# Performance work log

Measured on AMD Instinct MI355X. Metric: run time of the kernel, lower is better.

The kernel has to match this reference:

```python
import jax, jax.numpy as jnp
import numpy as np

T, B, IN, H = 1024, 128, 256, 512


def setup_inputs() -> dict:
    key = jax.random.key(0)
    k1, k2, k3, k4, k5 = jax.random.split(key, 5)
    s = 1.0 / np.sqrt(H)  # PyTorch LSTM init scale
    return {
        "x": jax.random.normal(k1, (T, B, IN), dtype=jnp.float32),
        "W_ih": jax.random.normal(k2, (4 * H, IN), dtype=jnp.float32) * s,
        "W_hh": jax.random.normal(k3, (4 * H, H), dtype=jnp.float32) * s,
        "b_ih": jax.random.normal(k4, (4 * H,), dtype=jnp.float32) * s,
        "b_hh": jax.random.normal(k5, (4 * H,), dtype=jnp.float32) * s,
    }


def reference(x, W_ih, W_hh, b_ih, b_hh):
    # Single-layer unidirectional LSTM scanned over the full sequence.
    # PyTorch gate order within the 4H dim: i, f, g, o.
    b = b_ih + b_hh
    Wx = jnp.einsum('tbi,gi->tbg', x, W_ih) + b  # precompute input projection [T,B,4H]

    def step(carry, zx):
        h, c = carry
        z = zx + h @ W_hh.T  # [B, 4H]
        i, f, g, o = jnp.split(z, 4, axis=-1)
        i = jax.nn.sigmoid(i)
        f = jax.nn.sigmoid(f)
        g = jnp.tanh(g)
        o = jax.nn.sigmoid(o)
        c = f * c + i * g
        h = o * jnp.tanh(c)
        return (h, c), None

    h0 = jnp.zeros((B, H), dtype=x.dtype)
    c0 = jnp.zeros((B, H), dtype=x.dtype)
    (h, c), _ = jax.lax.scan(step, (h0, c0), Wx)
    # Original returns the LAST step's output plus (h_n, c_n); with 1 layer output == h_n.
    output = h[None]          # [1, B, H]
    h_n = h[None]             # [num_layers=1, B, H]
    c_n = c[None]
    return (output, h_n, c_n)
```

## Files before the change

kernel.cpp:

```cpp
#include <hip/hip_runtime.h>
#include <hip/hip_bf16.h>

typedef __attribute__((ext_vector_type(8)))  short short8;
typedef __attribute__((ext_vector_type(16))) float f32x16;
typedef __attribute__((ext_vector_type(4)))  unsigned int uint4v;

#define TSTEPS 1024
#define BATCH  128
#define NIN    256
#define NHID   512
#define GM     4
#define GHB    16
#define MBLK   32
#define NHB    32
#define XSTR   264
#define HSTR   520

__device__ __forceinline__ unsigned short f2bf(float f) {
  unsigned int u = __builtin_bit_cast(unsigned int, f);
  u += 0x7fffu + ((u >> 16) & 1u);
  return (unsigned short)(u >> 16);
}

__device__ __forceinline__ unsigned long long pack4(float a, float b, float c, float d) {
  return (unsigned long long)f2bf(a)
       | ((unsigned long long)f2bf(b) << 16)
       | ((unsigned long long)f2bf(c) << 32)
       | ((unsigned long long)f2bf(d) << 48);
}

__device__ __forceinline__ float sigf(float x) {
  return 1.0f / (1.0f + __expf(-x));
}
__device__ __forceinline__ float tanh_fast(float x) {
  x = fminf(fmaxf(x, -15.0f), 15.0f);
  float e = __expf(2.0f * x);
  return (e - 1.0f) / (e + 1.0f);
}

__global__ void init_ws_kernel(unsigned long long* hbuf, unsigned int* flags) {
  int idx = blockIdx.x * blockDim.x + threadIdx.x;
  if (idx < 16384) hbuf[idx] = 0ull;
  if (idx < 8192) flags[idx] = 0u;
}

#define MFMA(va, fb, acc) \
  acc = __builtin_amdgcn_mfma_f32_32x32x16_bf16(va, fb, acc, 0, 0, 0)
#define AFRAG(base, kb) (*(const short8*)((base) + ((((kb) ^ x2) << 4) + (h5 << 3))))

__global__ __launch_bounds__(256, 1) void lstm_persistent(
    const float* __restrict__ x,
    const float* __restrict__ Wih,
    const float* __restrict__ Whh,
    const float* __restrict__ bih,
    const float* __restrict__ bhh,
    float* __restrict__ out,
    unsigned long long* __restrict__ hbuf,
    unsigned int* __restrict__ flags)
{
  const int tid  = threadIdx.x;
  const int lane = tid & 63;
  const int wv   = tid >> 6;
  const int gm   = blockIdx.x & (GM - 1);
  const int gh   = blockIdx.x >> 2;
  const int m0   = gm * MBLK;
  const int hc0  = gh * NHB;

  __shared__ short x_lds[2][MBLK][XSTR];
  __shared__ short h_lds[2][MBLK][HSTR];
  __shared__ float z_lds[4][MBLK][36];

  const int ncol = lane & 31;
  const int kg   = (lane >> 5) * 8;
  const int gate = ncol >> 3;
  const int wrow = gate * NHID + hc0 + wv * 8 + (ncol & 7);

  short8 bfrag[48];
#pragma unroll
  for (int kb = 0; kb < 48; ++kb) {
    const float* src = (kb < 16)
        ? (Wih + (size_t)wrow * NIN  + (kb * 16 + kg))
        : (Whh + (size_t)wrow * NHID + (kb * 16 + kg - NIN));
    float4 f0 = *(const float4*)src;
    float4 f1 = *(const float4*)(src + 4);
    short8 b;
    b[0] = (short)f2bf(f0.x); b[1] = (short)f2bf(f0.y);
    b[2] = (short)f2bf(f0.z); b[3] = (short)f2bf(f0.w);
    b[4] = (short)f2bf(f1.x); b[5] = (short)f2bf(f1.y);
    b[6] = (short)f2bf(f1.z); b[7] = (short)f2bf(f1.w);
    bfrag[kb] = b;
  }
  const float bias_c = bih[wrow] + bhh[wrow];

  const int h5   = lane >> 5;
  const int x2   = (lane >> 3) & 3;
  const int arow = lane & 31;
  const int grow = lane >> 1;
  const int gcol = (lane & 1) * 4;
  float creg[4] = {0.0f, 0.0f, 0.0f, 0.0f};

  unsigned int* fgrp   = flags + gm * (64 * 32);
  unsigned int* myflag = fgrp + (gh * 4 + wv) * 32;

#define XLOAD(i, v) { int u = tid + 256 * (i); \
    v = *(const float4*)(xt + (size_t)(u >> 6) * NIN + (u & 63) * 4); }
#define XPACK(s, i, v) { int u = tid + 256 * (i); int r = u >> 6; int hc = u & 63; \
    int off = ((((hc >> 1) ^ (((r >> 3) & 3) << 1))) << 3) + ((hc & 1) << 2); \
    *(unsigned long long*)&x_lds[s][r][off] = pack4(v.x, v.y, v.z, v.w); }

  f32x16 a0, a1, a2, a3;
  float4 xv0, xv1, xv2, xv3, xv4, xv5, xv6, xv7;

  {
    const float* xt = x + (size_t)m0 * NIN;
    XLOAD(0, xv0) XLOAD(1, xv1) XLOAD(2, xv2) XLOAD(3, xv3)
    XLOAD(4, xv4) XLOAD(5, xv5) XLOAD(6, xv6) XLOAD(7, xv7)
    XPACK(0, 0, xv0) XPACK(0, 1, xv1) XPACK(0, 2, xv2) XPACK(0, 3, xv3)
    XPACK(0, 4, xv4) XPACK(0, 5, xv5) XPACK(0, 6, xv6) XPACK(0, 7, xv7)
  }
  __syncthreads();
  {
    const float* xt = x + ((size_t)BATCH + m0) * NIN;
    XLOAD(0, xv0) XLOAD(1, xv1) XLOAD(2, xv2) XLOAD(3, xv3)
    XLOAD(4, xv4) XLOAD(5, xv5) XLOAD(6, xv6) XLOAD(7, xv7)
  }
  a0 = (f32x16)bias_c;
  a1 = (f32x16)0.0f; a2 = (f32x16)0.0f; a3 = (f32x16)0.0f;
  {
    const short* xrow = &x_lds[0][arow][0];
#pragma unroll
    for (int kb = 0; kb < 16; kb += 4) {
      MFMA(AFRAG(xrow, kb + 0), bfrag[kb + 0], a0);
      MFMA(AFRAG(xrow, kb + 1), bfrag[kb + 1], a1);
      MFMA(AFRAG(xrow, kb + 2), bfrag[kb + 2], a2);
      MFMA(AFRAG(xrow, kb + 3), bfrag[kb + 3], a3);
    }
  }
  XPACK(1, 0, xv0) XPACK(1, 1, xv1) XPACK(1, 2, xv2) XPACK(1, 3, xv3)
  XPACK(1, 4, xv4) XPACK(1, 5, xv5) XPACK(1, 6, xv6) XPACK(1, 7, xv7)

  for (int t = 0; t < TSTEPS; ++t) {
    if (t > 0) {
      const unsigned int* fp = fgrp + lane * 32;
      unsigned int v = __hip_atomic_load(fp, __ATOMIC_RELAXED, __HIP_MEMORY_SCOPE_AGENT);
      while (!__all((int)(v >= (unsigned int)t))) {
        v = __hip_atomic_load(fp, __ATOMIC_RELAXED, __HIP_MEMORY_SCOPE_AGENT);
      }
    }

    {
      const char* p =
          (const char*)(hbuf + (size_t)(t & 1) * 16384 + (size_t)m0 * 128) + tid * 16;
      uint4v hv0, hv1, hv2, hv3, hv4, hv5, hv6, hv7;
      asm volatile("global_load_dwordx4 %0, %1, off sc0 sc1" : "=v"(hv0) : "v"(p + 0 * 4096));
      asm volatile("global_load_dwordx4 %0, %1, off sc0 sc1" : "=v"(hv1) : "v"(p + 1 * 4096));
      asm volatile("global_load_dwordx4 %0, %1, off sc0 sc1" : "=v"(hv2) : "v"(p + 2 * 4096));
      asm volatile("global_load_dwordx4 %0, %1, off sc0 sc1" : "=v"(hv3) : "v"(p + 3 * 4096));
      asm volatile("global_load_dwordx4 %0, %1, off sc0 sc1" : "=v"(hv4) : "v"(p + 4 * 4096));
      asm volatile("global_load_dwordx4 %0, %1, off sc0 sc1" : "=v"(hv5) : "v"(p + 5 * 4096));
      asm volatile("global_load_dwordx4 %0, %1, off sc0 sc1" : "=v"(hv6) : "v"(p + 6 * 4096));
      asm volatile("global_load_dwordx4 %0, %1, off sc0 sc1" : "=v"(hv7) : "v"(p + 7 * 4096));
      asm volatile("s_waitcnt vmcnt(0)" ::: "memory");
      __builtin_amdgcn_sched_barrier(0);
#pragma unroll
      for (int i = 0; i < 8; ++i) {
        int r   = wv + 4 * i;
        int c16 = lane ^ (((r >> 3) & 3) << 1);
        uint4v v = (i == 0) ? hv0 : (i == 1) ? hv1 : (i == 2) ? hv2 : (i == 3) ? hv3
                 : (i == 4) ? hv4 : (i == 5) ? hv5 : (i == 6) ? hv6 : hv7;
        *(uint4v*)&h_lds[t & 1][r][c16 << 3] = v;
      }
    }
    __syncthreads();

    if (t + 2 < TSTEPS) {
      const float* xt = x + ((size_t)(t + 2) * BATCH + m0) * NIN;
      XLOAD(0, xv0) XLOAD(1, xv1) XLOAD(2, xv2) XLOAD(3, xv3)
      XLOAD(4, xv4) XLOAD(5, xv5) XLOAD(6, xv6) XLOAD(7, xv7)
    }

    {
      const short* hrow = &h_lds[t & 1][arow][0];
#pragma unroll
      for (int kb = 0; kb < 32; kb += 4) {
        MFMA(AFRAG(hrow, kb + 0), bfrag[16 + kb + 0], a0);
        MFMA(AFRAG(hrow, kb + 1), bfrag[16 + kb + 1], a1);
        MFMA(AFRAG(hrow, kb + 2), bfrag[16 + kb + 2], a2);
        MFMA(AFRAG(hrow, kb + 3), bfrag[16 + kb + 3], a3);
      }
    }

    {
      f32x16 acc = (a0 + a1) + (a2 + a3);
#pragma unroll
      for (int r = 0; r < 16; ++r) {
        int zr = (r & 3) + 8 * (r >> 2) + 4 * h5;
        z_lds[wv][zr][ncol] = acc[r];
      }
      asm volatile("s_waitcnt lgkmcnt(0)" ::: "memory");
      const float* zrow = &z_lds[wv][grow][0];
      float4 vi = *(const float4*)&zrow[ 0 + gcol];
      float4 vf = *(const float4*)&zrow[ 8 + gcol];
      float4 vg = *(const float4*)&zrow[16 + gcol];
      float4 vo = *(const float4*)&zrow[24 + gcol];
      float zi[4] = {vi.x, vi.y, vi.z, vi.w};
      float zf[4] = {vf.x, vf.y, vf.z, vf.w};
      float zg[4] = {vg.x, vg.y, vg.z, vg.w};
      float zo[4] = {vo.x, vo.y, vo.z, vo.w};
      float hnv[4];
#pragma unroll
      for (int u = 0; u < 4; ++u) {
        float iv = sigf(zi[u]);
        float fv = sigf(zf[u]);
        float gv = tanh_fast(zg[u]);
        float ov = sigf(zo[u]);
        float cn = fv * creg[u] + iv * gv;
        creg[u] = cn;
        hnv[u] = ov * tanh_fast(cn);
      }
      if (t == TSTEPS - 1) {
        size_t o = (size_t)(m0 + grow) * NHID + hc0 + wv * 8 + gcol;
        float4 hq; hq.x = hnv[0]; hq.y = hnv[1]; hq.z = hnv[2]; hq.w = hnv[3];
        float4 cq; cq.x = creg[0]; cq.y = creg[1]; cq.z = creg[2]; cq.w = creg[3];
        *(float4*)&out[o]          = hq;
        *(float4*)&out[65536 + o]  = hq;
        *(float4*)&out[131072 + o] = cq;
      } else {
        unsigned long long hp = pack4(hnv[0], hnv[1], hnv[2], hnv[3]);
        size_t hoff = (size_t)((t + 1) & 1) * 16384
                    + (size_t)(m0 + grow) * 128 + (hc0 + wv * 8 + gcol) / 4;
        __hip_atomic_store(hbuf + hoff, hp, __ATOMIC_RELAXED, __HIP_MEMORY_SCOPE_AGENT);
        asm volatile("s_waitcnt vmcnt(0)" ::: "memory");
        if (lane == 0) {
          __hip_atomic_store(myflag, (unsigned int)(t + 1),
                             __ATOMIC_RELAXED, __HIP_MEMORY_SCOPE_AGENT);
        }
      }
    }

    if (t + 2 < TSTEPS) {
      XPACK(t & 1, 0, xv0) XPACK(t & 1, 1, xv1) XPACK(t & 1, 2, xv2) XPACK(t & 1, 3, xv3)
      XPACK(t & 1, 4, xv4) XPACK(t & 1, 5, xv5) XPACK(t & 1, 6, xv6) XPACK(t & 1, 7, xv7)
    }

    if (t < TSTEPS - 1) {
      a0 = (f32x16)bias_c;
      a1 = (f32x16)0.0f; a2 = (f32x16)0.0f; a3 = (f32x16)0.0f;
      const short* xrow = &x_lds[(t + 1) & 1][arow][0];
#pragma unroll
      for (int kb = 0; kb < 16; kb += 4) {
        MFMA(AFRAG(xrow, kb + 0), bfrag[kb + 0], a0);
        MFMA(AFRAG(xrow, kb + 1), bfrag[kb + 1], a1);
        MFMA(AFRAG(xrow, kb + 2), bfrag[kb + 2], a2);
        MFMA(AFRAG(xrow, kb + 3), bfrag[kb + 3], a3);
      }
    }
  }
#undef XLOAD
#undef XPACK
}

extern "C" void kernel_launch(void* const* d_in, const int* in_sizes, int n_in,
                              void* d_out, int out_size, void* d_ws, size_t ws_size,
                              hipStream_t stream) {
  const float* x   = (const float*)d_in[0];
  const float* Wih = (const float*)d_in[1];
  const float* Whh = (const float*)d_in[2];
  const float* bih = (const float*)d_in[3];
  const float* bhh = (const float*)d_in[4];
  float* out = (float*)d_out;

  unsigned long long* hbuf = (unsigned long long*)d_ws;
  unsigned int* flags = (unsigned int*)((char*)d_ws + 262144);

  hipLaunchKernelGGL(init_ws_kernel, dim3(64), dim3(256), 0, stream, hbuf, flags);
  hipLaunchKernelGGL(lstm_persistent, dim3(64), dim3(256), 0, stream,
                     x, Wih, Whh, bih, bhh, out, hbuf, flags);
}
```

Baseline: 4.105 ms.

## Pre-convert x to bf16 and stream it into LDS with async DMA

Adds a pre-pass that converts x to bf16 in workspace, then loads each timestep's x tile straight into LDS with global_load_lds, using a triple buffer and a prefetch distance of three steps. This removes the per-step fp32 loads, register staging and bf16 packing from the recurrent loop. The gate nonlinearity is also remapped across all 256 threads, with a block barrier after the z write, and the LDS swizzles are dropped for plain strided layouts. Costs: an extra full pass over x, a new __syncthreads per step, and possible LDS bank conflicts from removing the swizzle.

```diff
diff --git a/kernel.cpp b/kernel.cpp
--- a/kernel.cpp
+++ b/kernel.cpp
@@ -10,11 +10,11 @@
 #define NIN    256
 #define NHID   512
 #define GM     4
-#define GHB    16
 #define MBLK   32
-#define NHB    32
-#define XSTR   264
+#define XPSTR  528
+#define XBUF   8448
 #define HSTR   520
+#define HBUF   16640
 
 __device__ __forceinline__ unsigned short f2bf(float f) {
   unsigned int u = __builtin_bit_cast(unsigned int, f);
@@ -44,12 +44,21 @@
   if (idx < 8192) flags[idx] = 0u;
 }
 
+__global__ void convert_x_kernel(const float* __restrict__ x, unsigned short* __restrict__ xbf) {
+  const int N4 = TSTEPS * BATCH * NIN / 4;
+  for (int i = blockIdx.x * blockDim.x + threadIdx.x; i < N4; i += gridDim.x * blockDim.x) {
+    float4 f = *(const float4*)(x + (size_t)i * 4);
+    *(unsigned long long*)(xbf + (size_t)i * 4) = pack4(f.x, f.y, f.z, f.w);
+  }
+}
+
 #define MFMA(va, fb, acc) \
   acc = __builtin_amdgcn_mfma_f32_32x32x16_bf16(va, fb, acc, 0, 0, 0)
-#define AFRAG(base, kb) (*(const short8*)((base) + ((((kb) ^ x2) << 4) + (h5 << 3))))
-
+
+template <int USE_DMA>
 __global__ __launch_bounds__(256, 1) void lstm_persistent(
     const float* __restrict__ x,
+    const unsigned short* __restrict__ xbf,
     const float* __restrict__ Wih,
     const float* __restrict__ Whh,
     const float* __restrict__ bih,
@@ -64,14 +73,16 @@
   const int gm   = blockIdx.x & (GM - 1);
   const int gh   = blockIdx.x >> 2;
   const int m0   = gm * MBLK;
-  const int hc0  = gh * NHB;
-
-  __shared__ short x_lds[2][MBLK][XSTR];
-  __shared__ short h_lds[2][MBLK][HSTR];
+  const int hc0  = gh * 32;
+
+  __shared__ short x_flat[3 * XBUF];
+  __shared__ short h_flat[2 * HBUF];
   __shared__ float z_lds[4][MBLK][36];
 
   const int ncol = lane & 31;
-  const int kg   = (lane >> 5) * 8;
+  const int h5   = lane >> 5;
+  const int arow = lane & 31;
+  const int kg   = h5 * 8;
   const int gate = ncol >> 3;
   const int wrow = gate * NHID + hc0 + wv * 8 + (ncol & 7);
 
@@ -92,11 +103,8 @@
   }
   const float bias_c = bih[wrow] + bhh[wrow];
 
-  const int h5   = lane >> 5;
-  const int x2   = (lane >> 3) & 3;
-  const int arow = lane & 31;
-  const int grow = lane >> 1;
-  const int gcol = (lane & 1) * 4;
+  const int grow = tid >> 3;
+  const int c4   = (tid & 7) * 4;
   float creg[4] = {0.0f, 0.0f, 0.0f, 0.0f};
 
   unsigned int* fgrp   = flags + gm * (64 * 32);
@@ -104,41 +112,52 @@
 
 #define XLOAD(i, v) { int u = tid + 256 * (i); \
     v = *(const float4*)(xt + (size_t)(u >> 6) * NIN + (u & 63) * 4); }
-#define XPACK(s, i, v) { int u = tid + 256 * (i); int r = u >> 6; int hc = u & 63; \
-    int off = ((((hc >> 1) ^ (((r >> 3) & 3) << 1))) << 3) + ((hc & 1) << 2); \
-    *(unsigned long long*)&x_lds[s][r][off] = pack4(v.x, v.y, v.z, v.w); }
+#define XPACK(bb, i, v) { int u = tid + 256 * (i); int r = u >> 6; int hc = u & 63; \
+    *(unsigned long long*)&x_flat[(bb) * XBUF + (r >> 1) * XPSTR + (r & 1) * NIN + hc * 4] \
+        = pack4(v.x, v.y, v.z, v.w); }
+#define XDMA(tt, bb) { \
+    const unsigned short* gsrc = xbf + ((size_t)(tt) * BATCH + m0) * NIN; \
+    short* ldst = x_flat + (bb) * XBUF; \
+    _Pragma("unroll") \
+    for (int j = 0; j < 4; ++j) { \
+      int ck = 4 * wv + j; \
+      const unsigned short* gp = gsrc + (size_t)(2 * ck + h5) * NIN + (lane & 31) * 8; \
+      __builtin_amdgcn_global_load_lds((const unsigned int*)gp, \
+          (unsigned int*)(ldst + ck * XPSTR), 16, 0, 0); \
+    } }
 
   f32x16 a0, a1, a2, a3;
   float4 xv0, xv1, xv2, xv3, xv4, xv5, xv6, xv7;
 
+  if (USE_DMA) {
+    XDMA(0, 0) XDMA(1, 1) XDMA(2, 2)
+    asm volatile("s_waitcnt vmcnt(0)" ::: "memory");
+  } else {
+    { const float* xt = x + (size_t)m0 * NIN;
+      XLOAD(0, xv0) XLOAD(1, xv1) XLOAD(2, xv2) XLOAD(3, xv3)
+      XLOAD(4, xv4) XLOAD(5, xv5) XLOAD(6, xv6) XLOAD(7, xv7)
+      XPACK(0, 0, xv0) XPACK(0, 1, xv1) XPACK(0, 2, xv2) XPACK(0, 3, xv3)
+      XPACK(0, 4, xv4) XPACK(0, 5, xv5) XPACK(0, 6, xv6) XPACK(0, 7, xv7) }
+    { const float* xt = x + ((size_t)BATCH + m0) * NIN;
+      XLOAD(0, xv0) XLOAD(1, xv1) XLOAD(2, xv2) XLOAD(3, xv3)
+      XLOAD(4, xv4) XLOAD(5, xv5) XLOAD(6, xv6) XLOAD(7, xv7)
+      XPACK(1, 0, xv0) XPACK(1, 1, xv1) XPACK(1, 2, xv2) XPACK(1, 3, xv3)
+      XPACK(1, 4, xv4) XPACK(1, 5, xv5) XPACK(1, 6, xv6) XPACK(1, 7, xv7) }
+  }
+  __syncthreads();
+  a0 = (f32x16)bias_c; a1 = (f32x16)0.0f; a2 = (f32x16)0.0f; a3 = (f32x16)0.0f;
   {
-    const float* xt = x + (size_t)m0 * NIN;
-    XLOAD(0, xv0) XLOAD(1, xv1) XLOAD(2, xv2) XLOAD(3, xv3)
-    XLOAD(4, xv4) XLOAD(5, xv5) XLOAD(6, xv6) XLOAD(7, xv7)
-    XPACK(0, 0, xv0) XPACK(0, 1, xv1) XPACK(0, 2, xv2) XPACK(0, 3, xv3)
-    XPACK(0, 4, xv4) XPACK(0, 5, xv5) XPACK(0, 6, xv6) XPACK(0, 7, xv7)
-  }
-  __syncthreads();
-  {
-    const float* xt = x + ((size_t)BATCH + m0) * NIN;
-    XLOAD(0, xv0) XLOAD(1, xv1) XLOAD(2, xv2) XLOAD(3, xv3)
-    XLOAD(4, xv4) XLOAD(5, xv5) XLOAD(6, xv6) XLOAD(7, xv7)
-  }
-  a0 = (f32x16)bias_c;
-  a1 = (f32x16)0.0f; a2 = (f32x16)0.0f; a3 = (f32x16)0.0f;
-  {
-    const short* xrow = &x_lds[0][arow][0];
+    const short* xrow = x_flat + (arow >> 1) * XPSTR + (arow & 1) * NIN + kg;
 #pragma unroll
     for (int kb = 0; kb < 16; kb += 4) {
-      MFMA(AFRAG(xrow, kb + 0), bfrag[kb + 0], a0);
-      MFMA(AFRAG(xrow, kb + 1), bfrag[kb + 1], a1);
-      MFMA(AFRAG(xrow, kb + 2), bfrag[kb + 2], a2);
-      MFMA(AFRAG(xrow, kb + 3), bfrag[kb + 3], a3);
-    }
-  }
-  XPACK(1, 0, xv0) XPACK(1, 1, xv1) XPACK(1, 2, xv2) XPACK(1, 3, xv3)
-  XPACK(1, 4, xv4) XPACK(1, 5, xv5) XPACK(1, 6, xv6) XPACK(1, 7, xv7)
-
+      MFMA(*(const short8*)(xrow + (kb + 0) * 16), bfrag[kb + 0], a0);
+      MFMA(*(const short8*)(xrow + (kb + 1) * 16), bfrag[kb + 1], a1);
+      MFMA(*(const short8*)(xrow + (kb + 2) * 16), bfrag[kb + 2], a2);
+      MFMA(*(const short8*)(xrow + (kb + 3) * 16), bfrag[kb + 3], a3);
+    }
+  }
+
+  int tmod = 0;
   for (int t = 0; t < TSTEPS; ++t) {
     if (t > 0) {
       const unsigned int* fp = fgrp + lane * 32;
@@ -162,31 +181,31 @@
       asm volatile("global_load_dwordx4 %0, %1, off sc0 sc1" : "=v"(hv7) : "v"(p + 7 * 4096));
       asm volatile("s_waitcnt vmcnt(0)" ::: "memory");
       __builtin_amdgcn_sched_barrier(0);
+      short* hdst = h_flat + (t & 1) * HBUF;
 #pragma unroll
       for (int i = 0; i < 8; ++i) {
-        int r   = wv + 4 * i;
-        int c16 = lane ^ (((r >> 3) & 3) << 1);
+        int r = wv + 4 * i;
         uint4v v = (i == 0) ? hv0 : (i == 1) ? hv1 : (i == 2) ? hv2 : (i == 3) ? hv3
                  : (i == 4) ? hv4 : (i == 5) ? hv5 : (i == 6) ? hv6 : hv7;
-        *(uint4v*)&h_lds[t & 1][r][c16 << 3] = v;
+        *(uint4v*)&hdst[r * HSTR + lane * 8] = v;
       }
     }
     __syncthreads();
 
-    if (t + 2 < TSTEPS) {
+    if (!USE_DMA && t + 2 < TSTEPS) {
       const float* xt = x + ((size_t)(t + 2) * BATCH + m0) * NIN;
       XLOAD(0, xv0) XLOAD(1, xv1) XLOAD(2, xv2) XLOAD(3, xv3)
       XLOAD(4, xv4) XLOAD(5, xv5) XLOAD(6, xv6) XLOAD(7, xv7)
     }
 
     {
-      const short* hrow = &h_lds[t & 1][arow][0];
+      const short* hrow = h_flat + (t & 1) * HBUF + arow * HSTR + kg;
 #pragma unroll
       for (int kb = 0; kb < 32; kb += 4) {
-        MFMA(AFRAG(hrow, kb + 0), bfrag[16 + kb + 0], a0);
-        MFMA(AFRAG(hrow, kb + 1), bfrag[16 + kb + 1], a1);
-        MFMA(AFRAG(hrow, kb + 2), bfrag[16 + kb + 2], a2);
-        MFMA(AFRAG(hrow, kb + 3), bfrag[16 + kb + 3], a3);
+        MFMA(*(const short8*)(hrow + (kb + 0) * 16), bfrag[16 + kb + 0], a0);
+        MFMA(*(const short8*)(hrow + (kb + 1) * 16), bfrag[16 + kb + 1], a1);
+        MFMA(*(const short8*)(hrow + (kb + 2) * 16), bfrag[16 + kb + 2], a2);
+        MFMA(*(const short8*)(hrow + (kb + 3) * 16), bfrag[16 + kb + 3], a3);
       }
     }
 
@@ -197,12 +216,17 @@
         int zr = (r & 3) + 8 * (r >> 2) + 4 * h5;
         z_lds[wv][zr][ncol] = acc[r];
       }
-      asm volatile("s_waitcnt lgkmcnt(0)" ::: "memory");
-      const float* zrow = &z_lds[wv][grow][0];
-      float4 vi = *(const float4*)&zrow[ 0 + gcol];
-      float4 vf = *(const float4*)&zrow[ 8 + gcol];
-      float4 vg = *(const float4*)&zrow[16 + gcol];
-      float4 vo = *(const float4*)&zrow[24 + gcol];
+    }
+    __syncthreads();
+
+    {
+      const int wz = c4 >> 3;
+      const int cc = c4 & 7;
+      const float* zrow = &z_lds[wz][grow][0];
+      float4 vi = *(const float4*)&zrow[ 0 + cc];
+      float4 vf = *(const float4*)&zrow[ 8 + cc];
+      float4 vg = *(const float4*)&zrow[16 + cc];
+      float4 vo = *(const float4*)&zrow[24 + cc];
       float zi[4] = {vi.x, vi.y, vi.z, vi.w};
       float zf[4] = {vf.x, vf.y, vf.z, vf.w};
       float zg[4] = {vg.x, vg.y, vg.z, vg.w};
@@ -219,7 +243,7 @@
         hnv[u] = ov * tanh_fast(cn);
       }
       if (t == TSTEPS - 1) {
-        size_t o = (size_t)(m0 + grow) * NHID + hc0 + wv * 8 + gcol;
+        size_t o = (size_t)(m0 + grow) * NHID + hc0 + c4;
         float4 hq; hq.x = hnv[0]; hq.y = hnv[1]; hq.z = hnv[2]; hq.w = hnv[3];
         float4 cq; cq.x = creg[0]; cq.y = creg[1]; cq.z = creg[2]; cq.w = creg[3];
         *(float4*)&out[o]          = hq;
@@ -228,8 +252,9 @@
       } else {
         unsigned long long hp = pack4(hnv[0], hnv[1], hnv[2], hnv[3]);
         size_t hoff = (size_t)((t + 1) & 1) * 16384
-                    + (size_t)(m0 + grow) * 128 + (hc0 + wv * 8 + gcol) / 4;
+                    + (size_t)(m0 + grow) * 128 + (hc0 + c4) / 4;
         __hip_atomic_store(hbuf + hoff, hp, __ATOMIC_RELAXED, __HIP_MEMORY_SCOPE_AGENT);
+        __builtin_amdgcn_sched_barrier(0);
         asm volatile("s_waitcnt vmcnt(0)" ::: "memory");
         if (lane == 0) {
           __hip_atomic_store(myflag, (unsigned int)(t + 1),
@@ -238,26 +263,30 @@
       }
     }
 
-    if (t + 2 < TSTEPS) {
-      XPACK(t & 1, 0, xv0) XPACK(t & 1, 1, xv1) XPACK(t & 1, 2, xv2) XPACK(t & 1, 3, xv3)
-      XPACK(t & 1, 4, xv4) XPACK(t & 1, 5, xv5) XPACK(t & 1, 6, xv6) XPACK(t & 1, 7, xv7)
-    }
-
     if (t < TSTEPS - 1) {
-      a0 = (f32x16)bias_c;
-      a1 = (f32x16)0.0f; a2 = (f32x16)0.0f; a3 = (f32x16)0.0f;
-      const short* xrow = &x_lds[(t + 1) & 1][arow][0];
+      if (USE_DMA) {
+        if (t + 3 < TSTEPS) { XDMA(t + 3, tmod) }
+      } else if (t + 2 < TSTEPS) {
+        int pb = tmod + 2; if (pb >= 3) pb -= 3;
+        XPACK(pb, 0, xv0) XPACK(pb, 1, xv1) XPACK(pb, 2, xv2) XPACK(pb, 3, xv3)
+        XPACK(pb, 4, xv4) XPACK(pb, 5, xv5) XPACK(pb, 6, xv6) XPACK(pb, 7, xv7)
+      }
+      int nb = tmod + 1; if (nb >= 3) nb -= 3;
+      a0 = (f32x16)bias_c; a1 = (f32x16)0.0f; a2 = (f32x16)0.0f; a3 = (f32x16)0.0f;
+      const short* xrow = x_flat + nb * XBUF + (arow >> 1) * XPSTR + (arow & 1) * NIN + kg;
 #pragma unroll
       for (int kb = 0; kb < 16; kb += 4) {
-        MFMA(AFRAG(xrow, kb + 0), bfrag[kb + 0], a0);
-        MFMA(AFRAG(xrow, kb + 1), bfrag[kb + 1], a1);
-        MFMA(AFRAG(xrow, kb + 2), bfrag[kb + 2], a2);
-        MFMA(AFRAG(xrow, kb + 3), bfrag[kb + 3], a3);
-      }
-    }
+        MFMA(*(const short8*)(xrow + (kb + 0) * 16), bfrag[kb + 0], a0);
+        MFMA(*(const short8*)(xrow + (kb + 1) * 16), bfrag[kb + 1], a1);
+        MFMA(*(const short8*)(xrow + (kb + 2) * 16), bfrag[kb + 2], a2);
+        MFMA(*(const short8*)(xrow + (kb + 3) * 16), bfrag[kb + 3], a3);
+      }
+    }
+    tmod = tmod + 1; if (tmod >= 3) tmod = 0;
   }
 #undef XLOAD
 #undef XPACK
+#undef XDMA
 }
 
 extern "C" void kernel_launch(void* const* d_in, const int* in_sizes, int n_in,
@@ -272,8 +301,18 @@
 
   unsigned long long* hbuf = (unsigned long long*)d_ws;
   unsigned int* flags = (unsigned int*)((char*)d_ws + 262144);
+  unsigned short* xbf = (unsigned short*)((char*)d_ws + (1 << 20));
+
+  size_t need = (size_t)(1 << 20) + (size_t)TSTEPS * BATCH * NIN * 2;
+  bool dma = ws_size >= need;
 
   hipLaunchKernelGGL(init_ws_kernel, dim3(64), dim3(256), 0, stream, hbuf, flags);
-  hipLaunchKernelGGL(lstm_persistent, dim3(64), dim3(256), 0, stream,
-                     x, Wih, Whh, bih, bhh, out, hbuf, flags);
-}
+  if (dma) {
+    hipLaunchKernelGGL(convert_x_kernel, dim3(8192), dim3(256), 0, stream, x, xbf);
+    hipLaunchKernelGGL((lstm_persistent<1>), dim3(64), dim3(256), 0, stream,
+                       x, xbf, Wih, Whh, bih, bhh, out, hbuf, flags);
+  } else {
+    hipLaunchKernelGGL((lstm_persistent<0>), dim3(64), dim3(256), 0, stream,
+                       x, xbf, Wih, Whh, bih, bhh, out, hbuf, flags);
+  }
+}
```

Measured after the change: 3.565 ms. 1.15x faster.
